# Optimization experiments

Measured on AMD Instinct MI355X. Metric: run time of the kernel, lower is better.

Reference implementation:

```python
import jax, jax.numpy as jnp
import numpy as np

N, T, CIN, F, HID, K, DIL, S = 10000, 64, 64, 64, 128, 3, 2, 8


def causal_temporal_block(h_ntc, W, b, dilation):
    # h_ntc: [N, T, Cin]; W: [Cout, Cin, K]. Conv1d with pad=(K-1)*d then chomp
    # of the trailing pad == left-only (causal) padding.
    pad = (W.shape[-1] - 1) * dilation
    h = jnp.transpose(h_ntc, (0, 2, 1))  # [N, Cin, T]
    y = jax.lax.conv_general_dilated(
        h, W, window_strides=(1,), padding=[(pad, 0)],
        rhs_dilation=(dilation,), dimension_numbers=("NCH", "OIH", "NCH"))
    y = jax.nn.relu(y + b[None, :, None])  # relu(relu(.)) == relu(.)
    return jnp.transpose(y, (0, 2, 1))  # [N, T, Cout]


def setup_inputs() -> dict:
    key = jax.random.key(0)
    ks = jax.random.split(key, 8)
    x = jax.random.normal(ks[0], (N, T, CIN), dtype=jnp.float32)
    W1 = jax.random.normal(ks[1], (F, CIN, K), dtype=jnp.float32) / np.sqrt(CIN * K)
    b1 = jnp.zeros((F,), dtype=jnp.float32)
    Wfc = jax.random.normal(ks[2], (HID, 2 * F), dtype=jnp.float32) / np.sqrt(2 * F)
    bfc = jnp.zeros((HID,), dtype=jnp.float32)
    W2 = jax.random.normal(ks[3], (F, HID, K), dtype=jnp.float32) / np.sqrt(HID * K)
    b2 = jnp.zeros((F,), dtype=jnp.float32)
    neighbor_idx = jax.random.randint(ks[4], (T, N, S), 0, N, dtype=jnp.int32)
    neighbor_mask = jnp.ones((T, N, S), dtype=bool)
    return {"x": x, "W1": W1, "b1": b1, "Wfc": Wfc, "bfc": bfc,
            "W2": W2, "b2": b2, "neighbor_idx": neighbor_idx,
            "neighbor_mask": neighbor_mask}


def reference(x, W1, b1, Wfc, bfc, W2, b2, neighbor_idx, neighbor_mask):
    # First temporal block
    h = causal_temporal_block(x, W1, b1, DIL)  # [N, T, F]

    # Per-timestep neighbor gather + masked mean aggregation
    h_t = jnp.transpose(h, (1, 0, 2))  # [T, N, F]
    gathered = jax.vmap(lambda ht, idx: ht[idx])(h_t, neighbor_idx)  # [T,N,S,F]
    m = neighbor_mask[..., None].astype(h.dtype)  # [T, N, S, 1]
    cnt = m.sum(axis=2)  # [T, N, 1]
    agg = (gathered * m).sum(axis=2) / jnp.maximum(cnt, 1.0)
    agg = jnp.where(cnt > 0, agg, h_t)  # fall back to self features
    agg = jnp.transpose(agg, (1, 0, 2))  # [N, T, F]

    # Combine self + aggregated neighbors, project, second temporal block
    combined = jnp.concatenate([h, agg], axis=-1)  # [N, T, 2F]
    out = jax.nn.relu(jnp.einsum("ntc,hc->nth", combined, Wfc) + bfc)
    out = causal_temporal_block(out, W2, b2, DIL)  # [N, T, F]
    # dropout: identity in eval mode
    return out
```

## Files before the change

### kernel.cpp

```cpp
#include <hip/hip_runtime.h>
#include <cstddef>
#include <cstdint>

#define NPTS 10000
#define TDIM 64
#define CINDIM 64
#define FDIM 64
#define HIDDIM 128
#define SDIM 8
#define NG 4
#define GNB 2000

typedef _Float16 f16;
typedef _Float16 f16x2 __attribute__((ext_vector_type(2)));
typedef _Float16 f16x4 __attribute__((ext_vector_type(4)));
typedef _Float16 f16x8 __attribute__((ext_vector_type(8)));
typedef float f32x4 __attribute__((ext_vector_type(4)));
typedef float f32x16 __attribute__((ext_vector_type(16)));

#define MFMA32(a, b, c) __builtin_amdgcn_mfma_f32_32x32x16_f16((a), (b), (c), 0, 0, 0)

static __device__ __forceinline__ f16x2 pk(float a, float b) {
  return __builtin_bit_cast(f16x2, __builtin_amdgcn_cvt_pkrtz(a, b));
}
static __device__ __forceinline__ f16x4 pack4(f32x4 p) {
  f16x2 h0 = pk(p[0], p[1]), h1 = pk(p[2], p[3]);
  return __builtin_shufflevector(h0, h1, 0, 1, 2, 3);
}
static __device__ __forceinline__ f16x4 pack4_relu(f32x4 v, f32x4 bias) {
  f16x4 r;
  r[0] = (f16)fmaxf(v[0] + bias[0], 0.f);
  r[1] = (f16)fmaxf(v[1] + bias[1], 0.f);
  r[2] = (f16)fmaxf(v[2] + bias[2], 0.f);
  r[3] = (f16)fmaxf(v[3] + bias[3], 0.f);
  return r;
}

__global__ __launch_bounds__(256) void prep_kernel(
    const float* __restrict__ W1, const float* __restrict__ Wfc,
    const float* __restrict__ W2, f16* __restrict__ w1h,
    f16* __restrict__ wfh, f16* __restrict__ w2h) {
  const int idx = blockIdx.x * 256 + threadIdx.x;
  const int j = idx & 7;
  if (idx < 2 * 12 * 512) {
    const int s = idx / 6144, rem = idx % 6144;
    const int ks = rem / 512, l = (rem % 512) >> 3;
    const int kk = ks * 16 + ((l >> 5) << 3) + j;
    const int k = kk >> 6, c = kk & 63, f = s * 32 + (l & 31);
    w1h[idx] = (f16)W1[f * 192 + c * 3 + k];
  }
  if (idx < 4 * 8 * 512) {
    const int s = idx / 4096, rem = idx % 4096;
    const int ks = rem / 512, l = (rem % 512) >> 3;
    const int kk = ks * 16 + ((l >> 5) << 3) + j;
    const int hc = s * 32 + (l & 31);
    wfh[idx] = (f16)Wfc[hc * 128 + kk];
  }
  if (idx < 2 * 24 * 512) {
    const int s = idx / 12288, rem = idx % 12288;
    const int ks = rem / 512, l = (rem % 512) >> 3;
    const int kk = ks * 16 + ((l >> 5) << 3) + j;
    const int k = kk >> 7, c = kk & 127, f = s * 32 + (l & 31);
    w2h[idx] = (f16)W2[f * 384 + c * 3 + k];
  }
}

__global__ __launch_bounds__(256) void conv1_kernel(
    const float* __restrict__ x, const f16* __restrict__ w1h,
    const float* __restrict__ b1, f16* __restrict__ h16t) {
  __shared__ f16 xs[68 * 72];
  const int tid = threadIdx.x;
  const int w = tid >> 6, lane = tid & 63;
  const int s = w >> 1, th = w & 1;
  const int rl = lane & 31, hi = lane >> 5;
  f16x8 wh[12];
#pragma unroll
  for (int ks = 0; ks < 12; ++ks)
    wh[ks] = *(const f16x8*)&w1h[((s * 12 + ks) * 64 + lane) * 8];
  f32x4 bias[4];
#pragma unroll
  for (int q = 0; q < 4; ++q) bias[q] = *(const f32x4*)&b1[s * 32 + 8 * q + 4 * hi];
  if (tid < 144) ((f16x2*)xs)[tid] = (f16x2){(f16)0, (f16)0};

  for (int g = 0; g < NG; ++g) {
    const int n = blockIdx.x * NG + g;
    const float* xn = x + (size_t)n * (TDIM * CINDIM);
    if (g) __syncthreads();
#pragma unroll
    for (int pass = 0; pass < 4; ++pass) {
      const int idx = pass * 256 + tid;
      const int row = idx >> 4, c4 = (idx & 15) * 4;
      const f32x4 v = *(const f32x4*)&xn[row * 64 + c4];
      *(f16x4*)&xs[(row + 4) * 72 + c4] = pack4(v);
    }
    __syncthreads();

    f32x16 acc;
#pragma unroll
    for (int i = 0; i < 16; ++i) acc[i] = 0.f;
#pragma unroll
    for (int ks = 0; ks < 12; ++ks) {
      const int k = ks >> 2;
      const int c0 = (ks & 3) * 16 + hi * 8;
      const f16x8 b = *(const f16x8*)&xs[(th * 32 + rl + 2 * k) * 72 + c0];
      acc = MFMA32(wh[ks], b, acc);
    }
    const int t = th * 32 + rl;
    f16* hrowt = h16t + ((size_t)t * NPTS + n) * 64;
#pragma unroll
    for (int q = 0; q < 4; ++q) {
      const f32x4 sub = {acc[4 * q], acc[4 * q + 1], acc[4 * q + 2], acc[4 * q + 3]};
      *(f16x4*)&hrowt[s * 32 + 8 * q + 4 * hi] = pack4_relu(sub, bias[q]);
    }
  }
}

__global__ __launch_bounds__(256) void gather_kernel(
    const f16* __restrict__ h16t, const int* __restrict__ nidx,
    const int* __restrict__ nmask, f16* __restrict__ agg16t) {
  const int tid = threadIdx.x;
  const int wv = tid >> 6, lane = tid & 63;
  const int oct = lane >> 3, sl8 = lane & 7;
  const int xcd = blockIdx.x & 7, q = blockIdx.x >> 3;
  const uint4* h128 = (const uint4*)h16t;
  uint4* agg128 = (uint4*)agg16t;

  int t = xcd * 8;
  int n = (q * 4 + wv) * 8;
  int ci, cm;
  {
    const size_t pr = ((size_t)t * NPTS + n) * SDIM;
    ci = nidx[pr + lane];
    cm = nmask[pr + lane];
  }
  for (int j = 0; j < 10; ++j) {
    int tn = t, nn = n + 8000;
    if (nn >= NPTS) { nn -= NPTS; ++tn; }
    int pi = 0, pm = 0;
    if (j + 1 < 10) {
      const size_t pr = ((size_t)tn * NPTS + nn) * SDIM;
      pi = nidx[pr + lane];
      pm = nmask[pr + lane];
    }
    const uint32_t tb = (uint32_t)t * (NPTS * 8) + sl8;
    uint4 u[8];
#pragma unroll
    for (int s = 0; s < SDIM; ++s) {
      const int is = __shfl(ci, oct * 8 + s, 64);
      u[s] = h128[tb + (uint32_t)is * 8u];
    }
    float a[8] = {0.f, 0.f, 0.f, 0.f, 0.f, 0.f, 0.f, 0.f};
    float cnt = 0.f;
#pragma unroll
    for (int s = 0; s < SDIM; ++s) {
      const float m = (__shfl(cm, oct * 8 + s, 64) != 0) ? 1.f : 0.f;
      const f16x2 p0 = __builtin_bit_cast(f16x2, u[s].x);
      const f16x2 p1 = __builtin_bit_cast(f16x2, u[s].y);
      const f16x2 p2 = __builtin_bit_cast(f16x2, u[s].z);
      const f16x2 p3 = __builtin_bit_cast(f16x2, u[s].w);
      a[0] = fmaf(m, (float)p0[0], a[0]);
      a[1] = fmaf(m, (float)p0[1], a[1]);
      a[2] = fmaf(m, (float)p1[0], a[2]);
      a[3] = fmaf(m, (float)p1[1], a[3]);
      a[4] = fmaf(m, (float)p2[0], a[4]);
      a[5] = fmaf(m, (float)p2[1], a[5]);
      a[6] = fmaf(m, (float)p3[0], a[6]);
      a[7] = fmaf(m, (float)p3[1], a[7]);
      cnt += m;
    }
    uint4 outv;
    if (cnt > 0.f) {
      const float inv = 1.f / cnt;
      const f16x4 lo4 = pack4((f32x4){a[0] * inv, a[1] * inv, a[2] * inv, a[3] * inv});
      const f16x4 hi4 = pack4((f32x4){a[4] * inv, a[5] * inv, a[6] * inv, a[7] * inv});
      const uint2 lo = __builtin_bit_cast(uint2, lo4);
      const uint2 hi = __builtin_bit_cast(uint2, hi4);
      outv.x = lo.x; outv.y = lo.y; outv.z = hi.x; outv.w = hi.y;
    } else {
      outv = h128[tb + (uint32_t)(n + oct) * 8u];
    }
    agg128[((size_t)t * NPTS + (n + oct)) * 8 + sl8] = outv;
    ci = pi; cm = pm; t = tn; n = nn;
  }
}

__global__ __launch_bounds__(256) void fc_conv2_kernel(
    const f16* __restrict__ h16t, const f16* __restrict__ agg16t,
    const f16* __restrict__ wfh, const float* __restrict__ bfc,
    const f16* __restrict__ w2h, const float* __restrict__ b2,
    float* __restrict__ out) {
  __shared__ f16 hs[64 * 72];
  __shared__ f16 as2[64 * 72];
  __shared__ f16 zs[68 * 136];
  const int tid = threadIdx.x;
  const int w = tid >> 6, lane = tid & 63;
  const int rl = lane & 31, hi = lane >> 5;
  f16x8 whf[8];
#pragma unroll
  for (int ks = 0; ks < 8; ++ks)
    whf[ks] = *(const f16x8*)&wfh[((w * 8 + ks) * 64 + lane) * 8];
  f32x4 biasf[4];
#pragma unroll
  for (int q = 0; q < 4; ++q)
    biasf[q] = *(const f32x4*)&bfc[w * 32 + 8 * q + 4 * hi];
  const int s2 = w >> 1, th2 = w & 1;
  f16x8 wh2[24];
#pragma unroll
  for (int ks = 0; ks < 24; ++ks)
    wh2[ks] = *(const f16x8*)&w2h[((s2 * 24 + ks) * 64 + lane) * 8];
  f32x4 bias2[4];
#pragma unroll
  for (int q = 0; q < 4; ++q)
    bias2[q] = *(const f32x4*)&b2[s2 * 32 + 8 * q + 4 * hi];
  if (tid < 136) ((f16x4*)zs)[tid] = (f16x4){(f16)0, (f16)0, (f16)0, (f16)0};

  for (int g = 0; g < NG; ++g) {
    const int n = blockIdx.x * NG + g;
    if (g) __syncthreads();
#pragma unroll
    for (int pass = 0; pass < 2; ++pass) {
      const int idx = pass * 256 + tid;
      const int row = idx >> 3, c8 = (idx & 7) * 8;
      *(f16x8*)&hs[row * 72 + c8] =
          *(const f16x8*)&h16t[((size_t)row * NPTS + n) * 64 + c8];
      *(f16x8*)&as2[row * 72 + c8] =
          *(const f16x8*)&agg16t[((size_t)row * NPTS + n) * 64 + c8];
    }
    __syncthreads();

#pragma unroll
    for (int tf = 0; tf < 2; ++tf) {
      f32x16 accf;
#pragma unroll
      for (int i = 0; i < 16; ++i) accf[i] = 0.f;
      const int t = tf * 32 + rl;
#pragma unroll
      for (int ks = 0; ks < 8; ++ks) {
        const int c0 = (ks & 3) * 16 + hi * 8;
        const f16x8 b = (ks < 4) ? *(const f16x8*)&hs[t * 72 + c0]
                                 : *(const f16x8*)&as2[t * 72 + c0];
        accf = MFMA32(whf[ks], b, accf);
      }
#pragma unroll
      for (int q = 0; q < 4; ++q) {
        const f32x4 sub = {accf[4 * q], accf[4 * q + 1], accf[4 * q + 2], accf[4 * q + 3]};
        *(f16x4*)&zs[(t + 4) * 136 + w * 32 + 8 * q + 4 * hi] =
            pack4_relu(sub, biasf[q]);
      }
    }
    __syncthreads();

    f32x16 acc;
#pragma unroll
    for (int i = 0; i < 16; ++i) acc[i] = 0.f;
#pragma unroll
    for (int ks = 0; ks < 24; ++ks) {
      const int k = ks >> 3;
      const int c0 = (ks & 7) * 16 + hi * 8;
      const f16x8 b = *(const f16x8*)&zs[(th2 * 32 + rl + 2 * k) * 136 + c0];
      acc = MFMA32(wh2[ks], b, acc);
    }
    const int t = th2 * 32 + rl;
    float* orow = out + ((size_t)n * 64 + t) * 64;
#pragma unroll
    for (int q = 0; q < 4; ++q) {
      f32x4 v;
      v[0] = fmaxf(acc[4 * q + 0] + bias2[q][0], 0.f);
      v[1] = fmaxf(acc[4 * q + 1] + bias2[q][1], 0.f);
      v[2] = fmaxf(acc[4 * q + 2] + bias2[q][2], 0.f);
      v[3] = fmaxf(acc[4 * q + 3] + bias2[q][3], 0.f);
      *(f32x4*)&orow[s2 * 32 + 8 * q + 4 * hi] = v;
    }
  }
}

extern "C" void kernel_launch(void* const* d_in, const int* in_sizes, int n_in,
                              void* d_out, int out_size, void* d_ws, size_t ws_size,
                              hipStream_t stream) {
  (void)in_sizes; (void)n_in; (void)out_size; (void)ws_size;
  const float* x   = (const float*)d_in[0];
  const float* W1  = (const float*)d_in[1];
  const float* b1  = (const float*)d_in[2];
  const float* Wfc = (const float*)d_in[3];
  const float* bfc = (const float*)d_in[4];
  const float* W2  = (const float*)d_in[5];
  const float* b2  = (const float*)d_in[6];
  const int* nidx  = (const int*)d_in[7];
  const int* nmask = (const int*)d_in[8];
  float* out = (float*)d_out;

  f16* wsf = (f16*)d_ws;
  f16* w1h = wsf;
  f16* wfh = w1h + 12288;
  f16* w2h = wfh + 16384;
  f16* h16t = w2h + 24576;
  f16* agg16t = h16t + (size_t)NPTS * TDIM * FDIM;

  prep_kernel<<<96, 256, 0, stream>>>(W1, Wfc, W2, w1h, wfh, w2h);
  conv1_kernel<<<NPTS / NG, 256, 0, stream>>>(x, w1h, b1, h16t);
  gather_kernel<<<GNB, 256, 0, stream>>>(h16t, nidx, nmask, agg16t);
  fc_conv2_kernel<<<NPTS / NG, 256, 0, stream>>>(h16t, agg16t, wfh, bfc,
                                                 w2h, b2, out);
}
```

Before: 217.8 us.

## Software-pipeline neighbor gathers and halve per-block work in conv1

The gather kernel now prefetches the next iteration's eight neighbor feature rows while the current ones are reduced, and loads indices two iterations ahead. Grid size is halved with twice as many iterations per wave to amortize that prefetch. conv1 processes two nodes per block instead of four, doubling its block count. This aims to hide gather latency and raise conv1 parallelism, at the cost of more registers in the gather kernel and more weight loads per node in conv1.

```diff
diff --git a/kernel.cpp b/kernel.cpp
--- a/kernel.cpp
+++ b/kernel.cpp
@@ -9,7 +9,10 @@
 #define HIDDIM 128
 #define SDIM 8
 #define NG 4
-#define GNB 2000
+#define CNG 2
+#define GNB 1000
+#define GJ 20
+#define GSTRIDE 4000
 
 typedef _Float16 f16;
 typedef _Float16 f16x2 __attribute__((ext_vector_type(2)));
@@ -82,8 +85,8 @@
   for (int q = 0; q < 4; ++q) bias[q] = *(const f32x4*)&b1[s * 32 + 8 * q + 4 * hi];
   if (tid < 144) ((f16x2*)xs)[tid] = (f16x2){(f16)0, (f16)0};
 
-  for (int g = 0; g < NG; ++g) {
-    const int n = blockIdx.x * NG + g;
+  for (int g = 0; g < CNG; ++g) {
+    const int n = blockIdx.x * CNG + g;
     const float* xn = x + (size_t)n * (TDIM * CINDIM);
     if (g) __syncthreads();
 #pragma unroll
@@ -125,29 +128,47 @@
   const uint4* h128 = (const uint4*)h16t;
   uint4* agg128 = (uint4*)agg16t;
 
-  int t = xcd * 8;
-  int n = (q * 4 + wv) * 8;
-  int ci, cm;
+  int t0 = xcd * 8;
+  int n0 = (q * 4 + wv) * 8;
+  int cm;
+  uint4 u[8];
   {
-    const size_t pr = ((size_t)t * NPTS + n) * SDIM;
-    ci = nidx[pr + lane];
+    const size_t pr = ((size_t)t0 * NPTS + n0) * SDIM;
+    const int ci = nidx[pr + lane];
     cm = nmask[pr + lane];
-  }
-  for (int j = 0; j < 10; ++j) {
-    int tn = t, nn = n + 8000;
-    if (nn >= NPTS) { nn -= NPTS; ++tn; }
-    int pi = 0, pm = 0;
-    if (j + 1 < 10) {
-      const size_t pr = ((size_t)tn * NPTS + nn) * SDIM;
-      pi = nidx[pr + lane];
-      pm = nmask[pr + lane];
-    }
-    const uint32_t tb = (uint32_t)t * (NPTS * 8) + sl8;
-    uint4 u[8];
+    const uint32_t tb = (uint32_t)t0 * (NPTS * 8) + sl8;
 #pragma unroll
     for (int s = 0; s < SDIM; ++s) {
       const int is = __shfl(ci, oct * 8 + s, 64);
       u[s] = h128[tb + (uint32_t)is * 8u];
+    }
+  }
+  int t1 = t0, n1 = n0 + GSTRIDE;
+  if (n1 >= NPTS) { n1 -= NPTS; ++t1; }
+  int ci1, cm1;
+  {
+    const size_t pr = ((size_t)t1 * NPTS + n1) * SDIM;
+    ci1 = nidx[pr + lane];
+    cm1 = nmask[pr + lane];
+  }
+
+  for (int j = 0; j < GJ; ++j) {
+    uint4 un[8];
+    if (j + 1 < GJ) {
+      const uint32_t tbn = (uint32_t)t1 * (NPTS * 8) + sl8;
+#pragma unroll
+      for (int s = 0; s < SDIM; ++s) {
+        const int is = __shfl(ci1, oct * 8 + s, 64);
+        un[s] = h128[tbn + (uint32_t)is * 8u];
+      }
+    }
+    int t2 = t1, n2 = n1 + GSTRIDE;
+    if (n2 >= NPTS) { n2 -= NPTS; ++t2; }
+    int ci2 = 0, cm2 = 0;
+    if (j + 2 < GJ) {
+      const size_t pr = ((size_t)t2 * NPTS + n2) * SDIM;
+      ci2 = nidx[pr + lane];
+      cm2 = nmask[pr + lane];
     }
     float a[8] = {0.f, 0.f, 0.f, 0.f, 0.f, 0.f, 0.f, 0.f};
     float cnt = 0.f;
@@ -177,10 +198,16 @@
       const uint2 hi = __builtin_bit_cast(uint2, hi4);
       outv.x = lo.x; outv.y = lo.y; outv.z = hi.x; outv.w = hi.y;
     } else {
-      outv = h128[tb + (uint32_t)(n + oct) * 8u];
-    }
-    agg128[((size_t)t * NPTS + (n + oct)) * 8 + sl8] = outv;
-    ci = pi; cm = pm; t = tn; n = nn;
+      const uint32_t tb = (uint32_t)t0 * (NPTS * 8) + sl8;
+      outv = h128[tb + (uint32_t)(n0 + oct) * 8u];
+    }
+    agg128[((size_t)t0 * NPTS + (n0 + oct)) * 8 + sl8] = outv;
+#pragma unroll
+    for (int s = 0; s < SDIM; ++s) u[s] = un[s];
+    cm = cm1;
+    t0 = t1; n0 = n1;
+    t1 = t2; n1 = n2;
+    ci1 = ci2; cm1 = cm2;
   }
 }
 
@@ -297,7 +324,7 @@
   f16* agg16t = h16t + (size_t)NPTS * TDIM * FDIM;
 
   prep_kernel<<<96, 256, 0, stream>>>(W1, Wfc, W2, w1h, wfh, w2h);
-  conv1_kernel<<<NPTS / NG, 256, 0, stream>>>(x, w1h, b1, h16t);
+  conv1_kernel<<<NPTS / CNG, 256, 0, stream>>>(x, w1h, b1, h16t);
   gather_kernel<<<GNB, 256, 0, stream>>>(h16t, nidx, nmask, agg16t);
   fc_conv2_kernel<<<NPTS / NG, 256, 0, stream>>>(h16t, agg16t, wfh, bfc,
                                                  w2h, b2, out);
```

New measurement: 217.1 us. About the same (-0.3%).
